# Performance work log

Measured on AMD Instinct MI355X. Metric: run time of the kernel, lower is better.

Reference implementation:

```python
import jax, jax.numpy as jnp
import numpy as np

B, C, W, H = 4, 256, 64, 64
N = W * H
SCALE = 0.02  # keep QK^T energies in a stable softmax range


def setup_inputs() -> dict:
    key = jax.random.key(0)
    ks = jax.random.split(key, 8)
    return {
        "x": jax.random.normal(ks[0], (B, C, W, H), jnp.float32),
        "geo_embed": jax.random.normal(ks[1], (B, N, C), jnp.float32),
        "Wq": jax.random.normal(ks[2], (C, C), jnp.float32) * SCALE,
        "bq": jnp.zeros((C,), jnp.float32),
        "Wk": jax.random.normal(ks[3], (C, C), jnp.float32) * SCALE,
        "bk": jnp.zeros((C,), jnp.float32),
        "Wv": jax.random.normal(ks[4], (C, C), jnp.float32) * SCALE,
        "bv": jnp.zeros((C,), jnp.float32),
        "Wgp": jax.random.normal(ks[5], (C, C), jnp.float32) * SCALE,
        "bgp": jnp.zeros((C,), jnp.float32),
        "Wgg": jax.random.normal(ks[6], (1, 2 * C), jnp.float32) * SCALE,
        "bgg": jnp.zeros((1,), jnp.float32),
    }


def reference(x, geo_embed, Wq, bq, Wk, bk, Wv, bv, Wgp, bgp, Wgg, bgg):
    b, c, w, h = x.shape
    n = w * h
    xf = x.reshape(b, c, n)  # [B, C, N]

    # 1x1 conv == per-pixel linear; q laid out [B, N, O] (permuted in torch)
    q = jnp.einsum("oc,bcn->bno", Wq, xf) + bq  # [B, N, O]

    # geo gating on the query
    ge = geo_embed @ Wgp.T + bgp  # [B, N, O]
    gate = jax.nn.sigmoid(jnp.concatenate([q, ge], axis=-1) @ Wgg.T + bgg)  # [B, N, 1]
    q = q + gate * ge

    k = jnp.einsum("oc,bcn->bon", Wk, xf) + bk[:, None]  # [B, O, N]
    v = jnp.einsum("oc,bcn->bon", Wv, xf) + bv[:, None]  # [B, C, N]

    energy = jnp.einsum("bno,bom->bnm", q, k)  # [B, N, N]
    attention = jax.nn.softmax(energy, axis=-1)

    # out = bmm(value, attention^T): out[b,c,m] = sum_n v[b,c,n] * attention[b,m,n]
    out = jnp.einsum("bcn,bmn->bcm", v, attention).reshape(b, c, w, h)

    # output gating: torch .view reinterpretation of (B, N, O) as (B, C, W, H)
    ge_r = ge.reshape(b, c, w, h)
    out = out * (1.0 + jax.nn.sigmoid(ge_r))
    return out, attention
```

## Files before the change

kernel.cpp:

```cpp
#include <hip/hip_runtime.h>
#include <hip/hip_bf16.h>
#include <math.h>

static constexpr int BB = 4;
static constexpr int CC = 256;
static constexpr int NN = 4096;

using bf16   = __bf16;
using f16    = _Float16;
using bf16x8 = __attribute__((ext_vector_type(8))) __bf16;
using bf16x4 = __attribute__((ext_vector_type(4))) __bf16;
using f16x8  = __attribute__((ext_vector_type(8))) _Float16;
using f16x4  = __attribute__((ext_vector_type(4))) _Float16;
using f32x4  = __attribute__((ext_vector_type(4))) float;

__device__ inline void gload_lds16(const void* g, void* l) {
  __builtin_amdgcn_global_load_lds(
      (const __attribute__((address_space(1))) void*)g,
      (__attribute__((address_space(3))) void*)l, 16, 0, 0);
}

__device__ inline void swz_bid(int& xb, int& yb, int& zb) {
  int gx = gridDim.x, gy = gridDim.y;
  int nwg = gx * gy * (int)gridDim.z;
  int flat = blockIdx.x + gx * (blockIdx.y + gy * blockIdx.z);
  int q = nwg >> 3;
  int w = (flat & 7) * q + (flat >> 3);
  xb = w % gx;
  int r = w / gx;
  yb = r % gy;
  zb = r / gy;
}

__global__ __launch_bounds__(256) void cvt_weights_kernel(
    const float* __restrict__ w0, const float* __restrict__ w1,
    const float* __restrict__ w2, const float* __restrict__ w3,
    bf16* __restrict__ out) {
  const float* srcs[4] = {w0, w1, w2, w3};
  const float* s = srcs[blockIdx.y];
  bf16* dst = out + (size_t)blockIdx.y * (CC * CC);
  int i = (blockIdx.x * 256 + threadIdx.x) * 4;
  float4 v = *(const float4*)(s + i);
  bf16x4 t;
  t[0] = (bf16)v.x; t[1] = (bf16)v.y; t[2] = (bf16)v.z; t[3] = (bf16)v.w;
  *(bf16x4*)(dst + i) = t;
}

__global__ __launch_bounds__(256) void transpose_x_kernel(
    const float* __restrict__ x, bf16* __restrict__ xt) {
  __shared__ float tile[64][65];
  int b  = blockIdx.z;
  int c0 = blockIdx.x * 64;
  int n0 = blockIdx.y * 64;
  const float* xp = x  + (long)b * CC * NN;
  bf16*       xtp = xt + (long)b * NN * CC;
  int tj = threadIdx.x & 63;
  int ti = threadIdx.x >> 6;
#pragma unroll
  for (int p = 0; p < 16; ++p) {
    int i = ti + p * 4;
    tile[i][tj] = xp[(long)(c0 + i) * NN + n0 + tj];
  }
  __syncthreads();
#pragma unroll
  for (int p = 0; p < 16; ++p) {
    int i = ti + p * 4;
    xtp[(long)(n0 + i) * CC + c0 + tj] = (bf16)tile[tj][i];
  }
}

__global__ __launch_bounds__(256) void proj_all_kernel(
    const bf16* __restrict__ xt, const float* __restrict__ geo,
    const bf16* __restrict__ Wall,
    const float* __restrict__ bq, const float* __restrict__ bgp,
    const float* __restrict__ bk, const float* __restrict__ bv,
    bf16* __restrict__ qn, f16* __restrict__ ge,
    bf16* __restrict__ kn, bf16* __restrict__ vb) {
  __shared__ bf16 As[128 * 32];
  __shared__ bf16 Bs[128 * 32];
  const long NCst = (long)NN * CC;
  const int bz = blockIdx.z;
  const int b = bz >> 2, p = bz & 3;
  const bf16 *Ap = nullptr, *Bp;
  const float* Af32 = nullptr;
  const float* bias;
  int row0, col0;
  if (p == 3) {
    Ap = Wall + 2 * CC * CC;
    Bp = xt + b * NCst;
    bias = bv;
    row0 = blockIdx.x * 128;
    col0 = blockIdx.y * 128;
  } else {
    if (p == 1) Af32 = geo + b * NCst;
    else        Ap   = xt + b * NCst;
    Bp = Wall + (size_t)(p == 0 ? 0 : (p == 1 ? 3 : 1)) * CC * CC;
    bias = (p == 0 ? bq : (p == 1 ? bgp : bk));
    row0 = blockIdx.y * 128;
    col0 = blockIdx.x * 128;
  }

  const int t   = threadIdx.x;
  const int wid = t >> 6;
  const int l   = t & 63;
  const int lr  = l & 15;
  const int lk  = (l >> 4) * 8;
  const int warow = (wid >> 1) * 64;
  const int wbcol = (wid & 1) * 64;
  const int srow = t >> 2;
  const int scol = (t & 3) * 8;
  const int frow = t >> 3;
  const int fc4  = (t & 7) * 4;

  f32x4 acc[4][4];
#pragma unroll
  for (int i = 0; i < 4; ++i)
#pragma unroll
    for (int j = 0; j < 4; ++j) acc[i][j] = {0.f, 0.f, 0.f, 0.f};

  for (int k0 = 0; k0 < CC; k0 += 32) {
    __syncthreads();
    if (p == 1) {
#pragma unroll
      for (int q = 0; q < 4; ++q) {
        float4 u = *(const float4*)(Af32 + (long)(row0 + frow + 32 * q) * CC + k0 + fc4);
        bf16x4 tv;
        tv[0] = (bf16)u.x; tv[1] = (bf16)u.y; tv[2] = (bf16)u.z; tv[3] = (bf16)u.w;
        *(bf16x4*)(As + (frow + 32 * q) * 32 + fc4) = tv;
      }
    } else {
#pragma unroll
      for (int q = 0; q < 2; ++q)
        gload_lds16(Ap + (long)(row0 + srow + 64 * q) * CC + k0 + scol,
                    As + ((q * 256 + t) * 8));
    }
#pragma unroll
    for (int q = 0; q < 2; ++q)
      gload_lds16(Bp + (long)(col0 + srow + 64 * q) * CC + k0 + scol,
                  Bs + ((q * 256 + t) * 8));
    __syncthreads();
    bf16x8 a[4], bb[4];
#pragma unroll
    for (int i = 0; i < 4; ++i)
      a[i] = *(const bf16x8*)(As + (warow + 16 * i + lr) * 32 + lk);
#pragma unroll
    for (int j = 0; j < 4; ++j)
      bb[j] = *(const bf16x8*)(Bs + (wbcol + 16 * j + lr) * 32 + lk);
#pragma unroll
    for (int i = 0; i < 4; ++i)
#pragma unroll
      for (int j = 0; j < 4; ++j)
        acc[i][j] = __builtin_amdgcn_mfma_f32_16x16x32_bf16(a[i], bb[j], acc[i][j], 0, 0, 0);
  }

  const int orow = (l >> 4) * 4;
  const int ocol = l & 15;
#pragma unroll
  for (int i = 0; i < 4; ++i) {
#pragma unroll
    for (int j = 0; j < 4; ++j) {
      int colb = col0 + wbcol + 16 * j + ocol;
#pragma unroll
      for (int r = 0; r < 4; ++r) {
        int row = row0 + warow + 16 * i + orow + r;
        if (p == 3) {
          float vv = acc[i][j][r] + bias[row];
          vb[b * NCst + (long)row * NN + colb] = (bf16)vv;
        } else {
          float vv = acc[i][j][r] + bias[colb];
          long di = b * NCst + (long)row * CC + colb;
          if (p == 1)
            ge[di] = (f16)vv;
          else
            (p == 0 ? qn : kn)[di] = (bf16)vv;
        }
      }
    }
  }
}

template <bool SWZ>
__global__ __launch_bounds__(512) void energy_kernel(
    const bf16* __restrict__ Q, const bf16* __restrict__ K,
    f16* __restrict__ E, float2* __restrict__ pstat) {
  __shared__ bf16 As[256 * 64];
  __shared__ bf16 Bs[128 * 64];
  __shared__ float2 sm[256][2];
  int bx = blockIdx.x, by = blockIdx.y, bz = blockIdx.z;
  if constexpr (SWZ) swz_bid(bx, by, bz);
  const long NCst = (long)NN * CC;
  const long NNst = (long)NN * NN;
  const bf16* Qb = Q + bz * NCst;
  const bf16* Kb = K + bz * NCst;
  f16* Eb = E + bz * NNst;
  const int row0 = by * 256;
  const int col0 = bx * 128;

  const int t   = threadIdx.x;
  const int wid = t >> 6;
  const int l   = t & 63;
  const int lr  = l & 15;
  const int lk8 = l >> 4;
  const int wm  = (wid >> 1) * 64;
  const int wn  = (wid & 1) * 64;

  const int srow = t >> 3;
  const int schk = t & 7;

  f32x4 acc[4][4];
#pragma unroll
  for (int i = 0; i < 4; ++i)
#pragma unroll
    for (int j = 0; j < 4; ++j) acc[i][j] = {0.f, 0.f, 0.f, 0.f};

  for (int k0 = 0; k0 < CC; k0 += 64) {
    __syncthreads();
#pragma unroll
    for (int p = 0; p < 4; ++p) {
      int r = srow + 64 * p;
      gload_lds16(Qb + (long)(row0 + r) * CC + k0 + ((schk ^ (r & 7)) * 8),
                  As + ((p * 512 + t) * 8));
    }
#pragma unroll
    for (int p = 0; p < 2; ++p) {
      int r = srow + 64 * p;
      gload_lds16(Kb + (long)(col0 + r) * CC + k0 + ((schk ^ (r & 7)) * 8),
                  Bs + ((p * 512 + t) * 8));
    }
    __syncthreads();
#pragma unroll
    for (int kk = 0; kk < 2; ++kk) {
      bf16x8 a[4], b[4];
#pragma unroll
      for (int i = 0; i < 4; ++i) {
        int Ra = wm + 16 * i + lr;
        a[i] = *(const bf16x8*)(As + Ra * 64 + (((kk * 4 + lk8) ^ (Ra & 7)) * 8));
      }
#pragma unroll
      for (int j = 0; j < 4; ++j) {
        int Rb = wn + 16 * j + lr;
        b[j] = *(const bf16x8*)(Bs + Rb * 64 + (((kk * 4 + lk8) ^ (Rb & 7)) * 8));
      }
#pragma unroll
      for (int i = 0; i < 4; ++i)
#pragma unroll
        for (int j = 0; j < 4; ++j)
          acc[i][j] = __builtin_amdgcn_mfma_f32_16x16x32_bf16(a[i], b[j], acc[i][j], 0, 0, 0);
    }
  }

  const int orow = (l >> 4) * 4;
  const int ocol = l & 15;
#pragma unroll
  for (int i = 0; i < 4; ++i) {
#pragma unroll
    for (int j = 0; j < 4; ++j) {
      int colb = col0 + wn + 16 * j + ocol;
#pragma unroll
      for (int r = 0; r < 4; ++r) {
        int row = row0 + wm + 16 * i + orow + r;
        Eb[(long)row * NN + colb] = (f16)acc[i][j][r];
      }
    }
  }

#pragma unroll
  for (int i = 0; i < 4; ++i) {
#pragma unroll
    for (int r = 0; r < 4; ++r) {
      float m = fmaxf(fmaxf(acc[i][0][r], acc[i][1][r]),
                      fmaxf(acc[i][2][r], acc[i][3][r]));
#pragma unroll
      for (int s = 8; s >= 1; s >>= 1) m = fmaxf(m, __shfl_xor(m, s, 64));
      float sum = 0.f;
#pragma unroll
      for (int j = 0; j < 4; ++j) sum += __expf(acc[i][j][r] - m);
#pragma unroll
      for (int s = 8; s >= 1; s >>= 1) sum += __shfl_xor(sum, s, 64);
      if ((l & 15) == 0) {
        int Rl = wm + 16 * i + (l >> 4) * 4 + r;
        sm[Rl][wid & 1] = make_float2(m, sum);
      }
    }
  }
  __syncthreads();
  if (t < 256) {
    float2 a2 = sm[t][0], b2 = sm[t][1];
    float m = fmaxf(a2.x, b2.x);
    float s = a2.y * __expf(a2.x - m) + b2.y * __expf(b2.x - m);
    pstat[((long)bz * NN + row0 + t) * 32 + bx] = make_float2(m, s);
  }
}

template <int BIAS_MODE, int B_MODE, int OUT_MODE, bool GATE_EPI, bool SWZ>
__global__ __launch_bounds__(256) void gemm_nt_lds(
    const bf16* __restrict__ A, const void* __restrict__ Bm,
    const float* __restrict__ bias, void* __restrict__ D,
    const f16* __restrict__ gefl,
    int Ncols, int K, long sA, long sB, long sD, long sGe) {
  __shared__ bf16 As[128 * 32];
  __shared__ bf16 Bs[128 * 32];
  int bx = blockIdx.x, by = blockIdx.y, bz = blockIdx.z;
  if constexpr (SWZ) swz_bid(bx, by, bz);
  const bf16* Ab = A + (long)bz * sA;
  const f16* geb = GATE_EPI ? (gefl + bz * sGe) : nullptr;

  const int t   = threadIdx.x;
  const int wid = t >> 6;
  const int l   = t & 63;
  const int lr  = l & 15;
  const int lk  = (l >> 4) * 8;
  const int row0 = by * 128;
  const int col0 = bx * 128;
  const int warow = (wid >> 1) * 64;
  const int wbcol = (wid & 1) * 64;

  const int srow = t >> 2;
  const int scol = (t & 3) * 8;
  const int frow = t >> 3;
  const int fc4  = (t & 7) * 4;

  f32x4 acc[4][4];
#pragma unroll
  for (int i = 0; i < 4; ++i)
#pragma unroll
    for (int j = 0; j < 4; ++j) acc[i][j] = {0.f, 0.f, 0.f, 0.f};

  for (int k0 = 0; k0 < K; k0 += 32) {
    __syncthreads();
#pragma unroll
    for (int p = 0; p < 2; ++p)
      gload_lds16(Ab + (long)(row0 + srow + 64 * p) * K + k0 + scol,
                  As + ((p * 256 + t) * 8));
    if constexpr (B_MODE == 0) {
      const bf16* Bb = (const bf16*)Bm + (long)bz * sB;
#pragma unroll
      for (int p = 0; p < 2; ++p)
        gload_lds16(Bb + (long)(col0 + srow + 64 * p) * K + k0 + scol,
                    Bs + ((p * 256 + t) * 8));
    } else {
      const float* Bf = (const float*)Bm + (long)bz * sB;
#pragma unroll
      for (int p = 0; p < 4; ++p) {
        float4 u = *(const float4*)(Bf + (long)(col0 + frow + 32 * p) * K + k0 + fc4);
        bf16x4 tv;
        tv[0] = (bf16)u.x; tv[1] = (bf16)u.y; tv[2] = (bf16)u.z; tv[3] = (bf16)u.w;
        *(bf16x4*)(Bs + (frow + 32 * p) * 32 + fc4) = tv;
      }
    }
    __syncthreads();
    bf16x8 a[4], bb[4];
#pragma unroll
    for (int i = 0; i < 4; ++i)
      a[i] = *(const bf16x8*)(As + (warow + 16 * i + lr) * 32 + lk);
#pragma unroll
    for (int j = 0; j < 4; ++j)
      bb[j] = *(const bf16x8*)(Bs + (wbcol + 16 * j + lr) * 32 + lk);
#pragma unroll
    for (int i = 0; i < 4; ++i)
#pragma unroll
      for (int j = 0; j < 4; ++j)
        acc[i][j] = __builtin_amdgcn_mfma_f32_16x16x32_bf16(a[i], bb[j], acc[i][j], 0, 0, 0);
  }

  const int orow = (l >> 4) * 4;
  const int ocol = l & 15;
#pragma unroll
  for (int i = 0; i < 4; ++i) {
#pragma unroll
    for (int j = 0; j < 4; ++j) {
      int colb = col0 + wbcol + 16 * j + ocol;
#pragma unroll
      for (int r = 0; r < 4; ++r) {
        int row = row0 + warow + 16 * i + orow + r;
        float vv = acc[i][j][r];
        if constexpr (BIAS_MODE == 1) vv += bias[colb];
        if constexpr (BIAS_MODE == 2) vv += bias[row];
        if constexpr (GATE_EPI) {
          float g = (float)geb[(long)row * 4096 + colb];
          vv *= 1.f + 1.f / (1.f + __expf(-g));
        }
        long di = bz * sD + (long)row * Ncols + colb;
        if constexpr (OUT_MODE == 0)
          ((float*)D)[di] = vv;
        else if constexpr (OUT_MODE == 1)
          ((bf16*)D)[di] = (bf16)vv;
        else
          ((f16*)D)[di] = (f16)vv;
      }
    }
  }
}

__global__ __launch_bounds__(256) void rowstat_reduce_kernel(
    const float2* __restrict__ pstat, float2* __restrict__ minv) {
  int row = blockIdx.x * 4 + (threadIdx.x >> 6);
  int l = threadIdx.x & 63;
  float2 v = (l < 32) ? pstat[(long)row * 32 + l] : make_float2(-1e30f, 0.f);
  float m = v.x;
#pragma unroll
  for (int s = 16; s >= 1; s >>= 1) m = fmaxf(m, __shfl_xor(m, s, 64));
  float sum = v.y * __expf(v.x - m);
#pragma unroll
  for (int s = 16; s >= 1; s >>= 1) sum += __shfl_xor(sum, s, 64);
  if (l == 0) minv[row] = make_float2(m, 1.f / sum);
}

template <bool SWZ>
__global__ __launch_bounds__(512) void pv_fused_kernel(
    const bf16* __restrict__ V, const f16* __restrict__ E,
    const float2* __restrict__ minv, float* __restrict__ attn,
    float* __restrict__ pbuf) {
  __shared__ bf16 Bs[2][64 * 64];
  int bx = blockIdx.x, by = blockIdx.y, bz = blockIdx.z;
  if constexpr (SWZ) swz_bid(bx, by, bz);
  const int mrow0 = bx * 64;
  const int KBASE = by * (NN / 2);
  const long NCst = (long)NN * CC;
  const long NNst = (long)NN * NN;
  const bf16* Vb = V + bz * NCst;
  const f16*  Eb = E + bz * NNst;
  float* attnb = attn + bz * NNst;
  float* pb = pbuf + (long)(bz * 2 + by) * NCst;

  const int t   = threadIdx.x;
  const int wid = t >> 6;
  const int l   = t & 63;
  const int lr  = l & 15;
  const int lk8 = l >> 4;
  const int crow = wid * 32;

  const int rE = t >> 3;
  const int q4 = (t & 7) * 4;
  const float2 mi = minv[(long)bz * NN + mrow0 + rE];
  const f16* Erow = Eb + (long)(mrow0 + rE) * NN + q4;
  float* Arow = attnb + (long)(mrow0 + rE) * NN + q4;
  const int c8a = (t & 7) >> 1;
  const int o4  = (t & 1) * 4;
  const int woff1 = rE * 64 + ((c8a ^ (rE & 7)) << 3) + o4;
  const int woff2 = rE * 64 + (((c8a + 4) ^ (rE & 7)) << 3) + o4;

  const bf16* Vr0 = Vb + (long)(crow + lr) * NN + lk8 * 8;
  const bf16* Vr1 = Vb + (long)(crow + 16 + lr) * NN + lk8 * 8;

  f32x4 acc[2][4];
#pragma unroll
  for (int i = 0; i < 2; ++i)
#pragma unroll
    for (int j = 0; j < 4; ++j) acc[i][j] = {0.f, 0.f, 0.f, 0.f};

  f16x4 elo = *(const f16x4*)(Erow + KBASE);
  f16x4 ehi = *(const f16x4*)(Erow + KBASE + 32);

  auto produce = [&](int kdst, int buf) {
    float pl[4], ph[4];
#pragma unroll
    for (int i = 0; i < 4; ++i) pl[i] = __expf((float)elo[i] - mi.x) * mi.y;
#pragma unroll
    for (int i = 0; i < 4; ++i) ph[i] = __expf((float)ehi[i] - mi.x) * mi.y;
    f32x4 u0 = {pl[0], pl[1], pl[2], pl[3]};
    f32x4 u1 = {ph[0], ph[1], ph[2], ph[3]};
    __builtin_nontemporal_store(u0, (f32x4*)(Arow + kdst));
    __builtin_nontemporal_store(u1, (f32x4*)(Arow + kdst + 32));
    bf16x4 b0, b1;
#pragma unroll
    for (int i = 0; i < 4; ++i) { b0[i] = (bf16)pl[i]; b1[i] = (bf16)ph[i]; }
    *(bf16x4*)(&Bs[buf][woff1]) = b0;
    *(bf16x4*)(&Bs[buf][woff2]) = b1;
    int kn = (kdst + 64) & (NN - 1);
    elo = *(const f16x4*)(Erow + kn);
    ehi = *(const f16x4*)(Erow + kn + 32);
  };

  auto consume = [&](int buf, bf16x8 a00, bf16x8 a01, bf16x8 a10, bf16x8 a11) {
    const bf16* B0 = &Bs[buf][0];
#pragma unroll
    for (int j = 0; j < 4; ++j) {
      int Rb = 16 * j + lr;
      bf16x8 b0 = *(const bf16x8*)(B0 + Rb * 64 + ((lk8 ^ (Rb & 7)) * 8));
      bf16x8 b1 = *(const bf16x8*)(B0 + Rb * 64 + (((lk8 + 4) ^ (Rb & 7)) * 8));
      acc[0][j] = __builtin_amdgcn_mfma_f32_16x16x32_bf16(a00, b0, acc[0][j], 0, 0, 0);
      acc[1][j] = __builtin_amdgcn_mfma_f32_16x16x32_bf16(a10, b0, acc[1][j], 0, 0, 0);
      acc[0][j] = __builtin_amdgcn_mfma_f32_16x16x32_bf16(a01, b1, acc[0][j], 0, 0, 0);
      acc[1][j] = __builtin_amdgcn_mfma_f32_16x16x32_bf16(a11, b1, acc[1][j], 0, 0, 0);
    }
  };

#define LOADV(k0, A0, A1, A2, A3)                  \
  A0 = *(const bf16x8*)(Vr0 + (k0));               \
  A1 = *(const bf16x8*)(Vr0 + (k0) + 32);          \
  A2 = *(const bf16x8*)(Vr1 + (k0));               \
  A3 = *(const bf16x8*)(Vr1 + (k0) + 32);

#define FENCE_BAR()                                         \
  asm volatile("s_waitcnt lgkmcnt(0)" ::: "memory");        \
  __builtin_amdgcn_s_barrier();                             \
  __builtin_amdgcn_sched_barrier(0);

  bf16x8 A00, A01, A10, A11, B00, B01, B10, B11;

  produce(KBASE, 0);
  LOADV(KBASE, A00, A01, A10, A11);
  FENCE_BAR();

  for (int it = 0; it < 15; ++it) {
    int k0 = KBASE + it * 128;
    LOADV(k0 + 64, B00, B01, B10, B11);
    consume(0, A00, A01, A10, A11);
    produce(k0 + 64, 1);
    FENCE_BAR();
    LOADV(k0 + 128, A00, A01, A10, A11);
    consume(1, B00, B01, B10, B11);
    produce(k0 + 128, 0);
    FENCE_BAR();
  }
  LOADV(KBASE + 1984, B00, B01, B10, B11);
  consume(0, A00, A01, A10, A11);
  produce(KBASE + 1984, 1);
  FENCE_BAR();
  consume(1, B00, B01, B10, B11);
#undef LOADV
#undef FENCE_BAR

  const int orow = (l >> 4) * 4;
  const int ocol = l & 15;
#pragma unroll
  for (int i = 0; i < 2; ++i) {
#pragma unroll
    for (int j = 0; j < 4; ++j) {
      int m = mrow0 + 16 * j + ocol;
#pragma unroll
      for (int r = 0; r < 4; ++r) {
        int c = crow + 16 * i + orow + r;
        __builtin_nontemporal_store(acc[i][j][r], pb + (long)c * 4096 + m);
      }
    }
  }
}

__global__ __launch_bounds__(256) void combine_kernel(
    const float* __restrict__ pbuf, const f16* __restrict__ ge,
    float* __restrict__ out) {
  const long NCst = (long)NN * CC;
  long i = ((long)blockIdx.x * 256 + threadIdx.x) * 8;
  int b = (int)(i >> 20);
  long r = i & (NCst - 1);
  const float* p0 = pbuf + (long)(b * 2) * NCst + r;
  const float* p1 = p0 + NCst;
  const f16* g = ge + (long)b * NCst + r;
  float* o = out + i;
  f16x8 gv = *(const f16x8*)(g);
#pragma unroll
  for (int h = 0; h < 2; ++h) {
    float4 a = *(const float4*)(p0 + h * 4);
    float4 c = *(const float4*)(p1 + h * 4);
    float4 u;
    u.x = (a.x + c.x) * (1.f + 1.f / (1.f + __expf(-(float)gv[4 * h + 0])));
    u.y = (a.y + c.y) * (1.f + 1.f / (1.f + __expf(-(float)gv[4 * h + 1])));
    u.z = (a.z + c.z) * (1.f + 1.f / (1.f + __expf(-(float)gv[4 * h + 2])));
    u.w = (a.w + c.w) * (1.f + 1.f / (1.f + __expf(-(float)gv[4 * h + 3])));
    *(float4*)(o + h * 4) = u;
  }
}

__global__ __launch_bounds__(256) void gate_kernel(
    bf16* __restrict__ q, const f16* __restrict__ ge,
    const float* __restrict__ Wgg, const float* __restrict__ bgg) {
  int row = blockIdx.x * 4 + (threadIdx.x >> 6);
  int l = threadIdx.x & 63;
  bf16* qr = q + (long)row * 256;
  const f16* ger = ge + (long)row * 256;
  float s = 0.f;
  float qv[4], gv[4];
#pragma unroll
  for (int i = 0; i < 4; ++i) {
    int o = l + 64 * i;
    qv[i] = (float)qr[o];
    gv[i] = (float)ger[o];
    s += qv[i] * Wgg[o] + gv[i] * Wgg[256 + o];
  }
#pragma unroll
  for (int m = 32; m >= 1; m >>= 1) s += __shfl_xor(s, m, 64);
  float gate = 1.f / (1.f + __expf(-(s + bgg[0])));
#pragma unroll
  for (int i = 0; i < 4; ++i) {
    int o = l + 64 * i;
    qr[o] = (bf16)(qv[i] + gate * gv[i]);
  }
}

__global__ __launch_bounds__(256) void softmax32_kernel(float* __restrict__ attn) {
  long row = blockIdx.x;
  float* p = attn + row * 4096;
  int t = threadIdx.x;
  __shared__ float red[8];
  float4 v[4];
  float mx = -1e30f;
#pragma unroll
  for (int c = 0; c < 4; ++c) {
    v[c] = *(const float4*)(p + c * 1024 + t * 4);
    mx = fmaxf(mx, fmaxf(fmaxf(v[c].x, v[c].y), fmaxf(v[c].z, v[c].w)));
  }
#pragma unroll
  for (int m = 32; m >= 1; m >>= 1) mx = fmaxf(mx, __shfl_xor(mx, m, 64));
  if ((t & 63) == 0) red[t >> 6] = mx;
  __syncthreads();
  mx = fmaxf(fmaxf(red[0], red[1]), fmaxf(red[2], red[3]));
  float sum = 0.f;
#pragma unroll
  for (int c = 0; c < 4; ++c) {
    v[c].x = __expf(v[c].x - mx);
    v[c].y = __expf(v[c].y - mx);
    v[c].z = __expf(v[c].z - mx);
    v[c].w = __expf(v[c].w - mx);
    sum += v[c].x + v[c].y + v[c].z + v[c].w;
  }
#pragma unroll
  for (int m = 32; m >= 1; m >>= 1) sum += __shfl_xor(sum, m, 64);
  if ((t & 63) == 0) red[4 + (t >> 6)] = sum;
  __syncthreads();
  float inv = 1.f / (red[4] + red[5] + red[6] + red[7]);
#pragma unroll
  for (int c = 0; c < 4; ++c) {
    v[c].x *= inv; v[c].y *= inv; v[c].z *= inv; v[c].w *= inv;
    *(float4*)(p + c * 1024 + t * 4) = v[c];
  }
}

extern "C" void kernel_launch(void* const* d_in, const int* in_sizes, int n_in,
                              void* d_out, int out_size, void* d_ws, size_t ws_size,
                              hipStream_t stream) {
  const float* x    = (const float*)d_in[0];
  const float* geo  = (const float*)d_in[1];
  const float* Wq   = (const float*)d_in[2];
  const float* bq   = (const float*)d_in[3];
  const float* Wk   = (const float*)d_in[4];
  const float* bk   = (const float*)d_in[5];
  const float* Wv   = (const float*)d_in[6];
  const float* bv   = (const float*)d_in[7];
  const float* Wgp  = (const float*)d_in[8];
  const float* bgp  = (const float*)d_in[9];
  const float* Wgg  = (const float*)d_in[10];
  const float* bgg  = (const float*)d_in[11];

  float* out  = (float*)d_out;
  float* attn = out + (long)BB * CC * NN;

  char* w = (char*)d_ws;
  size_t used = 0;
  auto alloc = [&](size_t bytes) {
    char* p = w + used;
    used += (bytes + 255) & ~(size_t)255;
    return p;
  };
  bf16*  xt   = (bf16*)alloc((size_t)BB * NN * CC * 2);
  bf16*  qn   = (bf16*)alloc((size_t)BB * NN * CC * 2);
  bf16*  kn   = (bf16*)alloc((size_t)BB * NN * CC * 2);
  bf16*  vb   = (bf16*)alloc((size_t)BB * CC * NN * 2);
  f16*   ge   = (f16*)alloc((size_t)BB * NN * CC * 2);
  bf16*  Wall = (bf16*)alloc((size_t)4 * CC * CC * 2);
  size_t abf_bytes   = (size_t)BB * NN * NN * 2;
  size_t pstat_bytes = (size_t)BB * NN * 32 * sizeof(float2);
  size_t minv_bytes  = (size_t)BB * NN * sizeof(float2);
  size_t pbuf_bytes  = (size_t)BB * 2 * NN * CC * 4;
  bool big = (ws_size >=
              used + abf_bytes + pstat_bytes + minv_bytes + pbuf_bytes + 2048);
  f16* abf = nullptr;
  float2* pstat = nullptr;
  float2* minv = nullptr;
  float* pbuf = nullptr;
  if (big) {
    abf   = (f16*)alloc(abf_bytes);
    pstat = (float2*)alloc(pstat_bytes);
    minv  = (float2*)alloc(minv_bytes);
    pbuf  = (float*)alloc(pbuf_bytes);
  }

  const long NCst = (long)NN * CC;
  const long NNst = (long)NN * NN;

  cvt_weights_kernel<<<dim3(64, 4), 256, 0, stream>>>(Wq, Wk, Wv, Wgp, Wall);
  transpose_x_kernel<<<dim3(4, 64, BB), 256, 0, stream>>>(x, xt);

  proj_all_kernel<<<dim3(2, 32, BB * 4), 256, 0, stream>>>(
      xt, geo, Wall, bq, bgp, bk, bv, qn, ge, kn, vb);
  gate_kernel<<<(BB * NN) / 4, 256, 0, stream>>>(qn, ge, Wgg, bgg);

  if (big) {
    energy_kernel<true><<<dim3(32, 16, BB), 512, 0, stream>>>(
        qn, kn, abf, pstat);
    rowstat_reduce_kernel<<<(BB * NN) / 4, 256, 0, stream>>>(pstat, minv);
    pv_fused_kernel<true><<<dim3(64, 2, BB), 512, 0, stream>>>(
        vb, abf, minv, attn, pbuf);
    combine_kernel<<<(int)((long)BB * NCst / (256 * 8)), 256, 0, stream>>>(
        pbuf, ge, out);
  } else {
    gemm_nt_lds<0, 0, 0, false, true><<<dim3(32, 32, BB), 256, 0, stream>>>(
        qn, kn, nullptr, attn, nullptr, NN, CC, NCst, NCst, NNst, 0);
    softmax32_kernel<<<BB * NN, 256, 0, stream>>>(attn);
    gemm_nt_lds<0, 1, 0, true, true><<<dim3(32, 2, BB), 256, 0, stream>>>(
        vb, attn, nullptr, out, ge, NN, NN, NCst, NNst, NCst, NCst);
  }
}
```

Before: 256.5 us.

## Fuse row-stat reduction into PV kernel and use nontemporal energy traffic

Removes the separate rowstat_reduce kernel. Each PV thread now merges the 32 partial (max, sum) pairs for its row with a small online-softmax merge and shuffles, instead of reading a precomputed minv buffer. The f16 energy stores in the energy kernel and the energy loads in the PV kernel become nontemporal hints, so the 128MB intermediate is meant to stream without polluting cache. The merge is now repeated by each of the 2×64 blocks' threads per row, adding a little redundant work, and nontemporal stores of scalar f16 may not coalesce as well.

New measurement: 309.8 us. 1.21x slower.

```diff
diff --git a/kernel.cpp b/kernel.cpp
--- a/kernel.cpp
+++ b/kernel.cpp
@@ -259,7 +259,7 @@
 #pragma unroll
       for (int r = 0; r < 4; ++r) {
         int row = row0 + wm + 16 * i + orow + r;
-        Eb[(long)row * NN + colb] = (f16)acc[i][j][r];
+        __builtin_nontemporal_store((f16)acc[i][j][r], Eb + (long)row * NN + colb);
       }
     }
   }
@@ -392,24 +392,10 @@
   }
 }
 
-__global__ __launch_bounds__(256) void rowstat_reduce_kernel(
-    const float2* __restrict__ pstat, float2* __restrict__ minv) {
-  int row = blockIdx.x * 4 + (threadIdx.x >> 6);
-  int l = threadIdx.x & 63;
-  float2 v = (l < 32) ? pstat[(long)row * 32 + l] : make_float2(-1e30f, 0.f);
-  float m = v.x;
-#pragma unroll
-  for (int s = 16; s >= 1; s >>= 1) m = fmaxf(m, __shfl_xor(m, s, 64));
-  float sum = v.y * __expf(v.x - m);
-#pragma unroll
-  for (int s = 16; s >= 1; s >>= 1) sum += __shfl_xor(sum, s, 64);
-  if (l == 0) minv[row] = make_float2(m, 1.f / sum);
-}
-
 template <bool SWZ>
 __global__ __launch_bounds__(512) void pv_fused_kernel(
     const bf16* __restrict__ V, const f16* __restrict__ E,
-    const float2* __restrict__ minv, float* __restrict__ attn,
+    const float2* __restrict__ pstat, float* __restrict__ attn,
     float* __restrict__ pbuf) {
   __shared__ bf16 Bs[2][64 * 64];
   int bx = blockIdx.x, by = blockIdx.y, bz = blockIdx.z;
@@ -432,7 +418,29 @@
 
   const int rE = t >> 3;
   const int q4 = (t & 7) * 4;
-  const float2 mi = minv[(long)bz * NN + mrow0 + rE];
+
+  float2 mi;
+  {
+    const float2* ps = pstat + ((long)bz * NN + mrow0 + rE) * 32 + (t & 7) * 4;
+    float m = -1e30f, s = 0.f;
+#pragma unroll
+    for (int i = 0; i < 4; ++i) {
+      float2 v = ps[i];
+      float mn = fmaxf(m, v.x);
+      s = s * __expf(m - mn) + v.y * __expf(v.x - mn);
+      m = mn;
+    }
+#pragma unroll
+    for (int msk = 1; msk <= 4; msk <<= 1) {
+      float om = __shfl_xor(m, msk, 64);
+      float os = __shfl_xor(s, msk, 64);
+      float mn = fmaxf(m, om);
+      s = s * __expf(m - mn) + os * __expf(om - mn);
+      m = mn;
+    }
+    mi = make_float2(m, 1.f / s);
+  }
+
   const f16* Erow = Eb + (long)(mrow0 + rE) * NN + q4;
   float* Arow = attnb + (long)(mrow0 + rE) * NN + q4;
   const int c8a = (t & 7) >> 1;
@@ -449,8 +457,8 @@
 #pragma unroll
     for (int j = 0; j < 4; ++j) acc[i][j] = {0.f, 0.f, 0.f, 0.f};
 
-  f16x4 elo = *(const f16x4*)(Erow + KBASE);
-  f16x4 ehi = *(const f16x4*)(Erow + KBASE + 32);
+  f16x4 elo = __builtin_nontemporal_load((const f16x4*)(Erow + KBASE));
+  f16x4 ehi = __builtin_nontemporal_load((const f16x4*)(Erow + KBASE + 32));
 
   auto produce = [&](int kdst, int buf) {
     float pl[4], ph[4];
@@ -468,8 +476,8 @@
     *(bf16x4*)(&Bs[buf][woff1]) = b0;
     *(bf16x4*)(&Bs[buf][woff2]) = b1;
     int kn = (kdst + 64) & (NN - 1);
-    elo = *(const f16x4*)(Erow + kn);
-    ehi = *(const f16x4*)(Erow + kn + 32);
+    elo = __builtin_nontemporal_load((const f16x4*)(Erow + kn));
+    ehi = __builtin_nontemporal_load((const f16x4*)(Erow + kn + 32));
   };
 
   auto consume = [&](int buf, bf16x8 a00, bf16x8 a01, bf16x8 a10, bf16x8 a11) {
@@ -661,18 +669,14 @@
   bf16*  Wall = (bf16*)alloc((size_t)4 * CC * CC * 2);
   size_t abf_bytes   = (size_t)BB * NN * NN * 2;
   size_t pstat_bytes = (size_t)BB * NN * 32 * sizeof(float2);
-  size_t minv_bytes  = (size_t)BB * NN * sizeof(float2);
   size_t pbuf_bytes  = (size_t)BB * 2 * NN * CC * 4;
-  bool big = (ws_size >=
-              used + abf_bytes + pstat_bytes + minv_bytes + pbuf_bytes + 2048);
+  bool big = (ws_size >= used + abf_bytes + pstat_bytes + pbuf_bytes + 2048);
   f16* abf = nullptr;
   float2* pstat = nullptr;
-  float2* minv = nullptr;
   float* pbuf = nullptr;
   if (big) {
     abf   = (f16*)alloc(abf_bytes);
     pstat = (float2*)alloc(pstat_bytes);
-    minv  = (float2*)alloc(minv_bytes);
     pbuf  = (float*)alloc(pbuf_bytes);
   }
 
@@ -689,9 +693,8 @@
   if (big) {
     energy_kernel<true><<<dim3(32, 16, BB), 512, 0, stream>>>(
         qn, kn, abf, pstat);
-    rowstat_reduce_kernel<<<(BB * NN) / 4, 256, 0, stream>>>(pstat, minv);
     pv_fused_kernel<true><<<dim3(64, 2, BB), 512, 0, stream>>>(
-        vb, abf, minv, attn, pbuf);
+        vb, abf, pstat, attn, pbuf);
     combine_kernel<<<(int)((long)BB * NCst / (256 * 8)), 256, 0, stream>>>(
         pbuf, ge, out);
   } else {
```
